# Kernel tuning notes

Hardware: AMD Instinct MI355X
Metric: run time of the kernel (lower is better)

## Reference

```python
import jax, jax.numpy as jnp
import numpy as np

B = 2048
D = 256
TEMPERATURE = 0.5
EPS = 1e-8  # torch.nn.CosineSimilarity eps


def _neg_indices(b):
    # Static mask: exclude diagonal and positive pairs (i, B+i), (B+i, i).
    n = 2 * b
    mask = np.ones((n, n), dtype=bool)
    np.fill_diagonal(mask, False)
    idx = np.arange(b)
    mask[idx, b + idx] = False
    mask[b + idx, idx] = False
    rows, cols = np.nonzero(mask)  # row-major order, matches torch sim[mask]
    return rows.reshape(n, n - 2), cols.reshape(n, n - 2)

_NEG_ROWS, _NEG_COLS = _neg_indices(B)


def setup_inputs() -> dict:
    key = jax.random.key(0)
    k1, k2 = jax.random.split(key)
    z_i = jax.random.normal(k1, (B, D), dtype=jnp.float32)
    z_j = jax.random.normal(k2, (B, D), dtype=jnp.float32)
    return {"z_i": z_i, "z_j": z_j}


def reference(z_i, z_j):
    b = z_i.shape[0]
    n = 2 * b
    z = jnp.concatenate([z_i, z_j], axis=0)  # [N, D]
    # Cosine similarity = normalize -> matmul (same math as broadcast CosineSimilarity)
    norm = jnp.maximum(jnp.linalg.norm(z, axis=1, keepdims=True), EPS)
    zn = z / norm
    sim = (zn @ zn.T) / TEMPERATURE  # [N, N]
    # positives: diag(sim, B) and diag(sim, -B)
    pos = jnp.concatenate([jnp.diagonal(sim, offset=b), jnp.diagonal(sim, offset=-b)], axis=0)  # [N]
    # negatives: static masked gather -> [N, N-2]
    neg = sim[_NEG_ROWS, _NEG_COLS]
    logits = jnp.concatenate([pos[:, None], neg], axis=1)  # [N, N-1]
    # CrossEntropyLoss(reduction='sum') with labels all zero, then / N
    loss = -jax.nn.log_softmax(logits, axis=1)[:, 0]
    return jnp.sum(loss) / n
```

## Files before the change

### kernel.cpp

```cpp
#include <hip/hip_runtime.h>
#include <hip/hip_bf16.h>
#include <math.h>

#define B_PAIRS 2048
#define N_ROWS  4096
#define D_DIM   256
#define INV_T   2.0f

typedef __attribute__((ext_vector_type(4))) float  floatx4;


__device__ __forceinline__ void async_copy16(const void* gsrc, void* ldst) {
    __builtin_amdgcn_global_load_lds(
        (__attribute__((address_space(1))) void*)gsrc,
        (__attribute__((address_space(3))) void*)ldst,
        16, 0, 0);
}

__global__ __launch_bounds__(256)
void ntx_normalize(const float* __restrict__ z_i,
                   const float* __restrict__ z_j,
                   unsigned* __restrict__ zn8t,
                   float* __restrict__ S,
                   float* __restrict__ posSum) {
    const int w    = threadIdx.x >> 6;
    const int lane = threadIdx.x & 63;
    const int row  = blockIdx.x * 4 + w;
    const float* src = (row < B_PAIRS) ? (z_i + (size_t)row * D_DIM)
                                       : (z_j + (size_t)(row - B_PAIRS) * D_DIM);
    const float4 v = *(const float4*)(src + lane * 4);
    float ss = v.x * v.x + v.y * v.y + v.z * v.z + v.w * v.w;
    #pragma unroll
    for (int off = 32; off > 0; off >>= 1) ss += __shfl_xor(ss, off, 64);
    const float rn = 1.0f / fmaxf(sqrtf(ss), 1e-8f);
    unsigned pk = 0;
    pk = __builtin_amdgcn_cvt_pk_fp8_f32(v.x * rn, v.y * rn, pk, false);
    pk = __builtin_amdgcn_cvt_pk_fp8_f32(v.z * rn, v.w * rn, pk, true);
    zn8t[(size_t)(lane >> 3) * 32768 + row * 8 + (lane & 7)] = pk;
    if (lane == 0) S[row] = 0.0f;
    if (blockIdx.x == 0 && threadIdx.x == 0) *posSum = 0.0f;
}

#define BM 128
#define BN 128
#define N_TILES 528

__global__ __launch_bounds__(256)
void ntx_simtile(const unsigned char* __restrict__ zn8t,
                 float* __restrict__ S,
                 float* __restrict__ posSum) {
    __shared__ __align__(16) unsigned char As[8 * 128 * 32];
    __shared__ __align__(16) unsigned char Bs[8 * 128 * 32];

    int t = blockIdx.x, by = 0, rowlen = 32;
    while (t >= rowlen) { t -= rowlen; by++; rowlen--; }
    const int bx = by + t;

    const int tid  = threadIdx.x;
    const int lane = tid & 63;
    const int w    = tid >> 6;
    const int wr   = w >> 1;
    const int wc   = w & 1;
    const int quad = lane >> 4;
    const int l16  = lane & 15;

    const int rowA0 = by * BM;
    const int rowB0 = bx * BN;
    const bool isDiag = (by == bx);
    const bool isPos  = (rowB0 == (rowA0 ^ B_PAIRS));

    #pragma unroll
    for (int s = 0; s < 8; s++) {
        async_copy16(zn8t + (size_t)s * 131072 + rowA0 * 32 + tid * 16,
                     As + s * 4096 + tid * 16);
        async_copy16(zn8t + (size_t)s * 131072 + rowB0 * 32 + tid * 16,
                     Bs + s * 4096 + tid * 16);
    }
    __syncthreads();

    floatx4 acc[4][4];
    #pragma unroll
    for (int i = 0; i < 4; i++)
        #pragma unroll
        for (int j = 0; j < 4; j++)
            acc[i][j] = (floatx4){0.f, 0.f, 0.f, 0.f};

    #pragma unroll
    for (int s = 0; s < 8; s++) {
        long afr[4], bfr[4];
        #pragma unroll
        for (int fi = 0; fi < 4; fi++) {
            const int ar = wr * 64 + fi * 16 + l16;
            afr[fi] = *(const long*)(const void*)(As + s * 4096 + ar * 32 + quad * 8);
        }
        #pragma unroll
        for (int fj = 0; fj < 4; fj++) {
            const int br = wc * 64 + fj * 16 + l16;
            bfr[fj] = *(const long*)(const void*)(Bs + s * 4096 + br * 32 + quad * 8);
        }
        #pragma unroll
        for (int fi = 0; fi < 4; fi++)
            #pragma unroll
            for (int fj = 0; fj < 4; fj++)
                acc[fi][fj] = __builtin_amdgcn_mfma_f32_16x16x32_fp8_fp8(
                    afr[fi], bfr[fj], acc[fi][fj], 0, 0, 0);
    }

    float cs[4] = {0.f, 0.f, 0.f, 0.f};
    float psum = 0.f;
    #pragma unroll
    for (int fi = 0; fi < 4; fi++) {
        float rs[4] = {0.f, 0.f, 0.f, 0.f};
        #pragma unroll
        for (int fj = 0; fj < 4; fj++) {
            const int rj = wc * 64 + fj * 16 + l16;
            #pragma unroll
            for (int reg = 0; reg < 4; reg++) {
                const int ri = wr * 64 + fi * 16 + quad * 4 + reg;
                const float v = acc[fi][fj][reg] * INV_T;
                const bool d = (ri == rj);
                if (isPos && d) psum += 2.0f * v;
                const float e = (isDiag && d) ? 0.f : __expf(v);
                rs[reg] += e;
                cs[fj]  += e;
            }
        }
        #pragma unroll
        for (int reg = 0; reg < 4; reg++) {
            float r = rs[reg];
            r += __shfl_xor(r, 1, 16);
            r += __shfl_xor(r, 2, 16);
            r += __shfl_xor(r, 4, 16);
            r += __shfl_xor(r, 8, 16);
            if (l16 == 0)
                atomicAdd(&S[rowA0 + wr * 64 + fi * 16 + quad * 4 + reg], r);
        }
    }
    if (!isDiag) {
        #pragma unroll
        for (int fj = 0; fj < 4; fj++) {
            float c = cs[fj];
            c += __shfl_xor(c, 16, 64);
            c += __shfl_xor(c, 32, 64);
            if (quad == 0)
                atomicAdd(&S[rowB0 + wc * 64 + fj * 16 + l16], c);
        }
    }
    if (isPos) {
        psum += __shfl_xor(psum, 1, 64);  psum += __shfl_xor(psum, 2, 64);
        psum += __shfl_xor(psum, 4, 64);  psum += __shfl_xor(psum, 8, 64);
        psum += __shfl_xor(psum, 16, 64); psum += __shfl_xor(psum, 32, 64);
        __shared__ float pred[4];
        if (lane == 0) pred[w] = psum;
        __syncthreads();
        if (tid == 0)
            atomicAdd(posSum, pred[0] + pred[1] + pred[2] + pred[3]);
    }
}

__global__ __launch_bounds__(1024)
void ntx_finalize(const float* __restrict__ S,
                  const float* __restrict__ posSum,
                  float* __restrict__ out) {
    const int tid = threadIdx.x;
    float acc = 0.f;
    #pragma unroll
    for (int c = 0; c < 4; c++)
        acc += __logf(S[tid + c * 1024]);
    #pragma unroll
    for (int off = 32; off > 0; off >>= 1) acc += __shfl_xor(acc, off, 64);
    __shared__ float red[16];
    if ((tid & 63) == 0) red[tid >> 6] = acc;
    __syncthreads();
    if (tid == 0) {
        float s = 0.f;
        #pragma unroll
        for (int k = 0; k < 16; k++) s += red[k];
        out[0] = (s - *posSum) / (float)N_ROWS;
    }
}

extern "C" void kernel_launch(void* const* d_in, const int* in_sizes, int n_in,
                              void* d_out, int out_size, void* d_ws, size_t ws_size,
                              hipStream_t stream) {
    const float* z_i = (const float*)d_in[0];
    const float* z_j = (const float*)d_in[1];
    float* out = (float*)d_out;

    unsigned char* zn8t = (unsigned char*)d_ws;
    float* S      = (float*)((char*)d_ws + (size_t)N_ROWS * D_DIM);
    float* posSum = S + N_ROWS;

    ntx_normalize<<<N_ROWS / 4, 256, 0, stream>>>(z_i, z_j, (unsigned*)zn8t, S, posSum);
    ntx_simtile<<<N_TILES, 256, 0, stream>>>(zn8t, S, posSum);
    ntx_finalize<<<1, 1024, 0, stream>>>(S, posSum, out);
}
```

Measured before the change: 77.10 us.

## Load fp8 fragments directly from global and fuse finalize via last-block counter

Removes the LDS staging of the A/B fp8 tiles: each wave now reads its MFMA fragments directly from global memory, relying on L2/L1 reuse, and the launch bounds ask for 4 blocks per CU. The separate finalize kernel is dropped. Instead, the last tile block to finish, found with an atomic done counter, computes the log-sum and writes the output. This saves one kernel launch and the LDS copy plus barrier, at the cost of uncoalesced 8-byte global loads and a serial tail in one block.

```diff
diff --git a/kernel.cpp b/kernel.cpp
--- a/kernel.cpp
+++ b/kernel.cpp
@@ -1,28 +1,21 @@
 #include <hip/hip_runtime.h>
-#include <hip/hip_bf16.h>
-#include <math.h>
 
 #define B_PAIRS 2048
 #define N_ROWS  4096
 #define D_DIM   256
 #define INV_T   2.0f
+#define N_TILES 528
 
-typedef __attribute__((ext_vector_type(4))) float  floatx4;
+typedef __attribute__((ext_vector_type(4))) float floatx4;
 
-
-__device__ __forceinline__ void async_copy16(const void* gsrc, void* ldst) {
-    __builtin_amdgcn_global_load_lds(
-        (__attribute__((address_space(1))) void*)gsrc,
-        (__attribute__((address_space(3))) void*)ldst,
-        16, 0, 0);
-}
 
 __global__ __launch_bounds__(256)
 void ntx_normalize(const float* __restrict__ z_i,
                    const float* __restrict__ z_j,
                    unsigned* __restrict__ zn8t,
                    float* __restrict__ S,
-                   float* __restrict__ posSum) {
+                   float* __restrict__ posSum,
+                   unsigned* __restrict__ done) {
     const int w    = threadIdx.x >> 6;
     const int lane = threadIdx.x & 63;
     const int row  = blockIdx.x * 4 + w;
@@ -38,19 +31,17 @@
     pk = __builtin_amdgcn_cvt_pk_fp8_f32(v.z * rn, v.w * rn, pk, true);
     zn8t[(size_t)(lane >> 3) * 32768 + row * 8 + (lane & 7)] = pk;
     if (lane == 0) S[row] = 0.0f;
-    if (blockIdx.x == 0 && threadIdx.x == 0) *posSum = 0.0f;
+    if (blockIdx.x == 0 && threadIdx.x == 0) { *posSum = 0.0f; *done = 0u; }
 }
 
-#define BM 128
-#define BN 128
-#define N_TILES 528
-
-__global__ __launch_bounds__(256)
+__global__ __launch_bounds__(256, 4)
 void ntx_simtile(const unsigned char* __restrict__ zn8t,
                  float* __restrict__ S,
-                 float* __restrict__ posSum) {
-    __shared__ __align__(16) unsigned char As[8 * 128 * 32];
-    __shared__ __align__(16) unsigned char Bs[8 * 128 * 32];
+                 float* __restrict__ posSum,
+                 unsigned* __restrict__ done,
+                 float* __restrict__ out) {
+    __shared__ float pred[4];
+    __shared__ int lastFlag;
 
     int t = blockIdx.x, by = 0, rowlen = 32;
     while (t >= rowlen) { t -= rowlen; by++; rowlen--; }
@@ -64,19 +55,13 @@
     const int quad = lane >> 4;
     const int l16  = lane & 15;
 
-    const int rowA0 = by * BM;
-    const int rowB0 = bx * BN;
+    const int rowA0 = by * 128;
+    const int rowB0 = bx * 128;
     const bool isDiag = (by == bx);
     const bool isPos  = (rowB0 == (rowA0 ^ B_PAIRS));
 
-    #pragma unroll
-    for (int s = 0; s < 8; s++) {
-        async_copy16(zn8t + (size_t)s * 131072 + rowA0 * 32 + tid * 16,
-                     As + s * 4096 + tid * 16);
-        async_copy16(zn8t + (size_t)s * 131072 + rowB0 * 32 + tid * 16,
-                     Bs + s * 4096 + tid * 16);
-    }
-    __syncthreads();
+    const size_t aoff = (size_t)(rowA0 + wr * 64 + l16) * 32 + quad * 8;
+    const size_t boff = (size_t)(rowB0 + wc * 64 + l16) * 32 + quad * 8;
 
     floatx4 acc[4][4];
     #pragma unroll
@@ -87,17 +72,15 @@
 
     #pragma unroll
     for (int s = 0; s < 8; s++) {
+        const unsigned char* bA = zn8t + (size_t)s * 131072 + aoff;
+        const unsigned char* bB = zn8t + (size_t)s * 131072 + boff;
         long afr[4], bfr[4];
         #pragma unroll
-        for (int fi = 0; fi < 4; fi++) {
-            const int ar = wr * 64 + fi * 16 + l16;
-            afr[fi] = *(const long*)(const void*)(As + s * 4096 + ar * 32 + quad * 8);
-        }
+        for (int fi = 0; fi < 4; fi++)
+            afr[fi] = *(const long*)(const void*)(bA + fi * 512);
         #pragma unroll
-        for (int fj = 0; fj < 4; fj++) {
-            const int br = wc * 64 + fj * 16 + l16;
-            bfr[fj] = *(const long*)(const void*)(Bs + s * 4096 + br * 32 + quad * 8);
-        }
+        for (int fj = 0; fj < 4; fj++)
+            bfr[fj] = *(const long*)(const void*)(bB + fj * 512);
         #pragma unroll
         for (int fi = 0; fi < 4; fi++)
             #pragma unroll
@@ -150,33 +133,36 @@
         psum += __shfl_xor(psum, 1, 64);  psum += __shfl_xor(psum, 2, 64);
         psum += __shfl_xor(psum, 4, 64);  psum += __shfl_xor(psum, 8, 64);
         psum += __shfl_xor(psum, 16, 64); psum += __shfl_xor(psum, 32, 64);
-        __shared__ float pred[4];
         if (lane == 0) pred[w] = psum;
         __syncthreads();
         if (tid == 0)
             atomicAdd(posSum, pred[0] + pred[1] + pred[2] + pred[3]);
     }
-}
 
-__global__ __launch_bounds__(1024)
-void ntx_finalize(const float* __restrict__ S,
-                  const float* __restrict__ posSum,
-                  float* __restrict__ out) {
-    const int tid = threadIdx.x;
-    float acc = 0.f;
-    #pragma unroll
-    for (int c = 0; c < 4; c++)
-        acc += __logf(S[tid + c * 1024]);
-    #pragma unroll
-    for (int off = 32; off > 0; off >>= 1) acc += __shfl_xor(acc, off, 64);
-    __shared__ float red[16];
-    if ((tid & 63) == 0) red[tid >> 6] = acc;
     __syncthreads();
     if (tid == 0) {
-        float s = 0.f;
-        #pragma unroll
-        for (int k = 0; k < 16; k++) s += red[k];
-        out[0] = (s - *posSum) / (float)N_ROWS;
+        __threadfence();
+        lastFlag = (atomicAdd(done, 1u) == N_TILES - 1) ? 1 : 0;
+    }
+    __syncthreads();
+    if (!lastFlag) return;
+    __threadfence();
+    float a = 0.f;
+    #pragma unroll
+    for (int c = 0; c < 16; c++) {
+        const float sv = __hip_atomic_load(&S[tid + c * 256],
+                                           __ATOMIC_RELAXED,
+                                           __HIP_MEMORY_SCOPE_AGENT);
+        a += __logf(sv);
+    }
+    #pragma unroll
+    for (int off = 32; off > 0; off >>= 1) a += __shfl_xor(a, off, 64);
+    if (lane == 0) pred[w] = a;
+    __syncthreads();
+    if (tid == 0) {
+        const float ps = __hip_atomic_load(posSum, __ATOMIC_RELAXED,
+                                           __HIP_MEMORY_SCOPE_AGENT);
+        out[0] = (pred[0] + pred[1] + pred[2] + pred[3] - ps) / (float)N_ROWS;
     }
 }
 
@@ -188,10 +174,11 @@
     float* out = (float*)d_out;
 
     unsigned char* zn8t = (unsigned char*)d_ws;
-    float* S      = (float*)((char*)d_ws + (size_t)N_ROWS * D_DIM);
-    float* posSum = S + N_ROWS;
+    float* S        = (float*)((char*)d_ws + (size_t)N_ROWS * D_DIM);
+    float* posSum   = S + N_ROWS;
+    unsigned* done  = (unsigned*)(posSum + 1);
 
-    ntx_normalize<<<N_ROWS / 4, 256, 0, stream>>>(z_i, z_j, (unsigned*)zn8t, S, posSum);
-    ntx_simtile<<<N_TILES, 256, 0, stream>>>(zn8t, S, posSum);
-    ntx_finalize<<<1, 1024, 0, stream>>>(S, posSum, out);
+    ntx_normalize<<<N_ROWS / 4, 256, 0, stream>>>(z_i, z_j, (unsigned*)zn8t,
+                                                  S, posSum, done);
+    ntx_simtile<<<N_TILES, 256, 0, stream>>>(zn8t, S, posSum, done, out);
 }
```

Result: slower. 80.28 us (+4.1%).
